# Kernel optimization log

Measured on AMD Instinct MI355X. Metric: run time of the kernel, lower is better.

Reference implementation:

```python
import jax, jax.numpy as jnp
import numpy as np

B, T, I, H, L = 128, 512, 64, 512, 64  # batch, seq_len, input=latent size, hidden
DEC_STEPS = 100  # hardcoded in the original decoder loop


def _lstm_cell(x, h, c, Wih, Whh, bih, bhh):
    # PyTorch gate order: i, f, g, o
    gates = x @ Wih.T + h @ Whh.T + bih + bhh  # [B, 4H]
    i, f, g, o = jnp.split(gates, 4, axis=-1)
    c = jax.nn.sigmoid(f) * c + jax.nn.sigmoid(i) * jnp.tanh(g)
    h = jax.nn.sigmoid(o) * jnp.tanh(c)
    return h, c


def setup_inputs() -> dict:
    key = jax.random.key(0)
    ks = jax.random.split(key, 18)
    u = lambda k, shape, fan: jax.random.uniform(k, shape, jnp.float32, -1.0, 1.0) / np.sqrt(fan).astype(np.float32)
    return {
        "sequences": jax.random.normal(ks[0], (B, T, I), jnp.float32),
        "seq_lengths": jnp.full((B,), T, dtype=jnp.int32),
        "eps": jax.random.normal(ks[1], (B, L), jnp.float32),
        "W_ih_enc": u(ks[2], (4 * H, I), H), "W_hh_enc": u(ks[3], (4 * H, H), H),
        "b_ih_enc": u(ks[4], (4 * H,), H), "b_hh_enc": u(ks[5], (4 * H,), H),
        "W_mean": u(ks[6], (L, H), H), "b_mean": u(ks[7], (L,), H),
        "W_logvar": u(ks[8], (L, H), H), "b_logvar": u(ks[9], (L,), H),
        "W_init": u(ks[10], (H, L), L), "b_init": u(ks[11], (H,), L),
        "W_ih_dec": u(ks[12], (4 * H, I), H), "W_hh_dec": u(ks[13], (4 * H, H), H),
        "b_ih_dec": u(ks[14], (4 * H,), H), "b_hh_dec": u(ks[15], (4 * H,), H),
        "W_out": u(ks[16], (I, H), H), "b_out": u(ks[17], (I,), H),
    }


def _forward(sequences, eps,
             W_ih_enc, W_hh_enc, b_ih_enc, b_hh_enc,
             W_mean, b_mean, W_logvar, b_logvar,
             W_init, b_init,
             W_ih_dec, W_hh_dec, b_ih_dec, b_hh_dec,
             W_out, b_out):
    Bn = sequences.shape[0]
    h0 = jnp.zeros((Bn, H), sequences.dtype)

    # ---- encoder: full-sequence LSTM, keep only final hidden state ----
    def enc_step(carry, x_t):
        h, c = carry
        h, c = _lstm_cell(x_t, h, c, W_ih_enc, W_hh_enc, b_ih_enc, b_hh_enc)
        return (h, c), None

    (h_n, _), _ = jax.lax.scan(enc_step, (h0, h0), sequences.transpose(1, 0, 2))

    # ---- VAE reparameterization ----
    mean = h_n @ W_mean.T + b_mean
    log_var = h_n @ W_logvar.T + b_logvar
    z = mean + eps * jnp.exp(0.5 * log_var)

    h_dec = z @ W_init.T + b_init
    c_dec = jnp.zeros_like(h_dec)
    x0 = jnp.zeros((Bn, L), z.dtype)

    def dec_step(carry, _):
        h, c, x = carry
        h, c = _lstm_cell(x, h, c, W_ih_dec, W_hh_dec, b_ih_dec, b_hh_dec)
        x_hat = h @ W_out.T + b_out
        return (h, c, x_hat), x_hat

    _, xs = jax.lax.scan(dec_step, (h_dec, c_dec, x0), None, length=DEC_STEPS)
    x_hat = xs.transpose(1, 0, 2)  # [B, 100, I]
    return x_hat, mean, log_var


def reference(sequences, seq_lengths, eps,
              W_ih_enc, W_hh_enc, b_ih_enc, b_hh_enc,
              W_mean, b_mean, W_logvar, b_logvar,
              W_init, b_init,
              W_ih_dec, W_hh_dec, b_ih_dec, b_hh_dec,
              W_out, b_out):
    del seq_lengths  # accepted but unused by the original forward
    return _forward(sequences, eps,
                    W_ih_enc, W_hh_enc, b_ih_enc, b_hh_enc,
                    W_mean, b_mean, W_logvar, b_logvar,
                    W_init, b_init,
                    W_ih_dec, W_hh_dec, b_ih_dec, b_hh_dec,
                    W_out, b_out)
```

## Files before the change

### kernel.cpp

```cpp
#include <hip/hip_runtime.h>
#include <stdint.h>


typedef short short8 __attribute__((ext_vector_type(8)));
typedef float f32x4 __attribute__((ext_vector_type(4)));
typedef unsigned int u32x4 __attribute__((ext_vector_type(4)));

#define WS_FLAGS  0
#define WS_HBUF0  16384
#define WS_HBUF1  147456
#define WS_Z      278528
#define WS_BCOMB  311296
#define WS_WCOMB  319488
#define WS_SEQB   2416640
#define WS_END    10805248
#define WS_ZERO   WS_HBUF1

static __device__ __forceinline__ float b2f(unsigned short u) {
    return __builtin_bit_cast(float, (unsigned int)u << 16);
}
static __device__ __forceinline__ unsigned short f2b(float f) {
    unsigned int u = __builtin_bit_cast(unsigned int, f);
    unsigned int r = u + 0x7FFFu + ((u >> 16) & 1u);
    return (unsigned short)(r >> 16);
}
static __device__ __forceinline__ float sigm(float x)  { return 1.0f / (1.0f + __expf(-x)); }
static __device__ __forceinline__ float tanhx(float x) { return 1.0f - 2.0f / (__expf(2.0f * x) + 1.0f); }

static __device__ __forceinline__ short8 cvt8(const float* p) {
    const float4 a = ((const float4*)p)[0];
    const float4 b = ((const float4*)p)[1];
    short8 r;
    r[0] = (short)f2b(a.x); r[1] = (short)f2b(a.y);
    r[2] = (short)f2b(a.z); r[3] = (short)f2b(a.w);
    r[4] = (short)f2b(b.x); r[5] = (short)f2b(b.y);
    r[6] = (short)f2b(b.z); r[7] = (short)f2b(b.w);
    return r;
}

static __device__ __forceinline__ void load2x16_cc(const void* p0, const void* p1,
                                                   u32x4& v0, u32x4& v1) {
    asm volatile("global_load_dwordx4 %0, %2, off sc0 sc1\n\t"
                 "global_load_dwordx4 %1, %3, off sc0 sc1\n\t"
                 "s_waitcnt vmcnt(0)"
                 : "=&v"(v0), "=&v"(v1) : "v"(p0), "v"(p1) : "memory");
}
static __device__ __forceinline__ void store16_cc(void* p, u32x4 v) {
    asm volatile("global_store_dwordx4 %0, %1, off sc0 sc1"
                 :: "v"(p), "v"(v) : "memory");
}
static __device__ __forceinline__ void drain_vm() {
    asm volatile("s_waitcnt vmcnt(0)" ::: "memory");
}

__global__ void __launch_bounds__(256)
seqcvt_kernel(const float* __restrict__ src, unsigned short* __restrict__ dst)
{
    int i = (blockIdx.x * 256 + threadIdx.x) * 4;
    float4 v = *(const float4*)(src + i);
    uint32_t lo = (uint32_t)f2b(v.x) | ((uint32_t)f2b(v.y) << 16);
    uint32_t hi = (uint32_t)f2b(v.z) | ((uint32_t)f2b(v.w) << 16);
    uint2 o; o.x = lo; o.y = hi;
    *(uint2*)(dst + i) = o;
}

__global__ void __launch_bounds__(256)
wcomb_kernel(const float* __restrict__ Wih_d,
             const float* __restrict__ Whh_d,
             const float* __restrict__ Wout,
             const float* __restrict__ bih_d,
             const float* __restrict__ bhh_d,
             const float* __restrict__ bout,
             unsigned char* __restrict__ ws)
{
    __shared__ float Ash[64][64];
    __shared__ float Bsh[64][65];
    const int bid = blockIdx.x, t = threadIdx.x;
    const int gt0 = (bid >> 3) * 64, ht0 = (bid & 7) * 64;
    for (int j = 0; j < 16; ++j) {
        int idx = t + j * 256;
        int r = idx >> 6, c = idx & 63;
        Ash[r][c] = Wih_d[(size_t)(gt0 + r) * 64 + c];
        Bsh[r][c] = Wout[(size_t)r * 512 + ht0 + c];
    }
    __syncthreads();
    const int gl = t >> 2, hl0 = (t & 3) * 16;
    for (int hh = 0; hh < 16; ++hh) {
        float acc = 0.f;
        #pragma unroll
        for (int i = 0; i < 64; ++i) acc += Ash[gl][i] * Bsh[i][hl0 + hh];
        int g = gt0 + gl, h = ht0 + hl0 + hh;
        float v = Whh_d[(size_t)g * 512 + h] + acc;
        ((unsigned short*)(ws + WS_WCOMB))[(size_t)g * 512 + h] = f2b(v);
    }
    if ((bid & 7) == 0 && t < 64) {
        int g = gt0 + t;
        float acc = bih_d[g] + bhh_d[g];
        #pragma unroll
        for (int i = 0; i < 64; ++i) acc += bout[i] * Ash[t][i];
        ((float*)(ws + WS_BCOMB))[g] = acc;
    }
}

__global__ void __launch_bounds__(512, 2)
vae_persistent(const float* __restrict__ seq,
               const unsigned short* __restrict__ seqb,
               const float* __restrict__ eps,
               const float* __restrict__ Wih_e,
               const float* __restrict__ Whh_e,
               const float* __restrict__ bih_e,
               const float* __restrict__ bhh_e,
               const float* __restrict__ Wmean,
               const float* __restrict__ bmean,
               const float* __restrict__ Wlv,
               const float* __restrict__ blv,
               const float* __restrict__ Winit,
               const float* __restrict__ binit,
               const float* __restrict__ Whh_d,
               const float* __restrict__ bih_d,
               const float* __restrict__ bhh_d,
               const float* __restrict__ Wout,
               const float* __restrict__ bout,
               unsigned char* __restrict__ ws,
               float* __restrict__ out)
{
    __shared__ __align__(16) short Al[16 * 520];
    __shared__ __align__(16) short Ho[512];
    __shared__ float fbuf[128];
    __shared__ float zl[16 * 64];

    const int tid  = threadIdx.x;
    const int g    = blockIdx.x & 7;
    const int s    = blockIdx.x >> 3;
    const int b0   = g * 16;
    const int lane = tid & 63;
    const int wv   = tid >> 6;
    const int col  = lane & 15;
    const int q    = lane >> 4;
    const int nloc = wv * 16 + col;
    const int gt   = nloc & 3;
    const int grow = gt * 512 + s * 32 + (nloc >> 2);

    uint32_t* flags = (uint32_t*)(ws + WS_FLAGS) + (size_t)g * 512;
    unsigned char* hbuf0 = ws + WS_HBUF0;
    unsigned char* hbuf1 = ws + WS_HBUF1;
    uint32_t* zbuf = (uint32_t*)(ws + WS_Z);

    float cst[4] = {0.f, 0.f, 0.f, 0.f};

    auto wait_and_stage = [&](uint32_t R) {
        if (wv == 0 && lane < 16) {
            while (__hip_atomic_load(&flags[lane * 32], __ATOMIC_RELAXED,
                                     __HIP_MEMORY_SCOPE_AGENT) < R) {}
        }
        __syncthreads();
        const unsigned char* src = (R & 1) ? hbuf1 : hbuf0;
        const int b = tid >> 5, c = tid & 31;
        const unsigned char* p0 = src + (size_t)(b0 + b) * 1024 + c * 32;
        u32x4 v0, v1;
        load2x16_cc(p0, p0 + 16, v0, v1);
        u32x4* dst = (u32x4*)Al;
        dst[b * 65 + c * 2 + 0] = v0;
        dst[b * 65 + c * 2 + 1] = v1;
        __syncthreads();
    };

    auto publish_h = [&](uint32_t R) {
        if (wv == 0) {
            unsigned char* dst = (R & 1) ? hbuf1 : hbuf0;
            int row = lane >> 2, part = lane & 3;
            u32x4 v = ((const u32x4*)Ho)[lane];
            store16_cc(dst + (size_t)(b0 + row) * 1024 + s * 64 + part * 16, v);
            drain_vm();
            if (lane == 0)
                __hip_atomic_store(&flags[s * 32], R, __ATOMIC_RELAXED,
                                   __HIP_MEMORY_SCOPE_AGENT);
        }
    };

    short8 wfrag[16];
    auto load_wfrag_f32 = [&](const float* Wsrc) {
        #pragma unroll
        for (int kt = 0; kt < 16; ++kt)
            wfrag[kt] = cvt8(Wsrc + (size_t)grow * 512 + kt * 32 + q * 8);
    };
    auto load_wfrag_bf16 = [&](const unsigned short* Wsrc) {
        #pragma unroll
        for (int kt = 0; kt < 16; ++kt)
            wfrag[kt] = *(const short8*)((const short*)Wsrc +
                         (size_t)grow * 512 + kt * 32 + q * 8);
    };

    auto cell_update = [&](f32x4 acc) {
        float act[4];
        #pragma unroll
        for (int r = 0; r < 4; ++r)
            act[r] = (gt == 2) ? tanhx(acc[r]) : sigm(acc[r]);
        int base = lane & ~3;
        #pragma unroll
        for (int r = 0; r < 4; ++r) {
            float vi = __shfl(act[r], base + 0);
            float vf = __shfl(act[r], base + 1);
            float vg = __shfl(act[r], base + 2);
            float vo = __shfl(act[r], base + 3);
            cst[r] = vf * cst[r] + vi * vg;
            act[r] = vo * tanhx(cst[r]);
        }
        if (gt == 0) {
            int hd4 = wv * 4 + (col >> 2);
            #pragma unroll
            for (int r = 0; r < 4; ++r)
                Ho[(q * 4 + r) * 32 + hd4] = (short)f2b(act[r]);
        }
    };

    load_wfrag_f32(Whh_e);
    short8 xwf[2];
    #pragma unroll
    for (int kt = 0; kt < 2; ++kt)
        xwf[kt] = cvt8(Wih_e + (size_t)grow * 64 + kt * 32 + q * 8);
    const float bias_e = bih_e[grow] + bhh_e[grow];

    auto load_x = [&](int t, short8* xf) {
        if (seqb) {
            const short* xs = (const short*)seqb + ((size_t)(b0 + col) * 512 + t) * 64 + q * 8;
            xf[0] = *(const short8*)(xs);
            xf[1] = *(const short8*)(xs + 32);
        } else {
            const float* xs = seq + ((size_t)(b0 + col) * 512 + t) * 64 + q * 8;
            xf[0] = cvt8(xs);
            xf[1] = cvt8(xs + 32);
        }
    };

    short8 xf[2];
    load_x(0, xf);
    for (uint32_t t = 0; t < 512; ++t) {
        wait_and_stage(t);
        f32x4 acc = {bias_e, bias_e, bias_e, bias_e};
        acc = __builtin_amdgcn_mfma_f32_16x16x32_bf16(xf[0], xwf[0], acc, 0, 0, 0);
        acc = __builtin_amdgcn_mfma_f32_16x16x32_bf16(xf[1], xwf[1], acc, 0, 0, 0);
        if (t < 511) load_x(t + 1, xf);
        #pragma unroll
        for (int kt = 0; kt < 16; ++kt) {
            short8 a = *(const short8*)(Al + col * 520 + kt * 32 + q * 8);
            acc = __builtin_amdgcn_mfma_f32_16x16x32_bf16(a, wfrag[kt], acc, 0, 0, 0);
        }
        cell_update(acc);
        __syncthreads();
        publish_h(t + 1);
    }

    wait_and_stage(512);
    if (tid < 128) {
        int which = tid >> 6, idx = tid & 63;
        int b = idx >> 2, ldl = idx & 3;
        int ld = s * 4 + ldl;
        const float* wrow = (which ? Wlv : Wmean) + (size_t)ld * 512;
        float a = (which ? blv[ld] : bmean[ld]);
        for (int k = 0; k < 512; ++k)
            a += b2f((unsigned short)Al[b * 520 + k]) * wrow[k];
        out[819200 + which * 8192 + (size_t)(b0 + b) * 64 + ld] = a;
        fbuf[which * 64 + idx] = a;
    }
    __syncthreads();
    if (wv == 0) {
        int b = lane >> 2, ldl = lane & 3;
        int ld = s * 4 + ldl;
        float m = fbuf[lane], lv = fbuf[64 + lane];
        float e = eps[(size_t)(b0 + b) * 64 + ld];
        float z = m + e * __expf(0.5f * lv);
        __hip_atomic_store(zbuf + (size_t)(b0 + b) * 64 + ld,
                           __builtin_bit_cast(uint32_t, z),
                           __ATOMIC_RELAXED, __HIP_MEMORY_SCOPE_AGENT);
        drain_vm();
        if (lane == 0)
            __hip_atomic_store(&flags[s * 32], 513u,
                               __ATOMIC_RELAXED, __HIP_MEMORY_SCOPE_AGENT);
    }
    if (wv == 0 && lane < 16)
        while (__hip_atomic_load(&flags[lane * 32], __ATOMIC_RELAXED,
                                 __HIP_MEMORY_SCOPE_AGENT) < 513u) {}
    __syncthreads();

    #pragma unroll
    for (int j = 0; j < 2; ++j) {
        int idx = tid + j * 512;
        int b = idx >> 6, l = idx & 63;
        uint32_t v = __hip_atomic_load(zbuf + (size_t)(b0 + b) * 64 + l,
                                       __ATOMIC_RELAXED, __HIP_MEMORY_SCOPE_AGENT);
        zl[b * 64 + l] = __builtin_bit_cast(float, v);
    }
    __syncthreads();
    {
        int b = tid >> 5, c = tid & 31;
        #pragma unroll
        for (int j = 0; j < 16; ++j) {
            int hd = c * 16 + j;
            float a = binit[hd];
            const float* wr = Winit + (size_t)hd * 64;
            #pragma unroll
            for (int l = 0; l < 64; ++l) a += zl[b * 64 + l] * wr[l];
            Al[b * 520 + hd] = (short)f2b(a);
        }
    }
    #pragma unroll
    for (int r = 0; r < 4; ++r) cst[r] = 0.f;
    __syncthreads();

    short8 wof[16];
    float xbias = 0.f;
    if (s < 4 && wv == 7) {
        xbias = bout[s * 16 + col];
        #pragma unroll
        for (int kt = 0; kt < 16; ++kt)
            wof[kt] = cvt8(Wout + (size_t)(s * 16 + col) * 512 + kt * 32 + q * 8);
    }
    auto xhat_emit = [&](int d) {
        f32x4 a2 = {xbias, xbias, xbias, xbias};
        #pragma unroll
        for (int kt = 0; kt < 16; ++kt) {
            short8 a = *(const short8*)(Al + col * 520 + kt * 32 + q * 8);
            a2 = __builtin_amdgcn_mfma_f32_16x16x32_bf16(a, wof[kt], a2, 0, 0, 0);
        }
        #pragma unroll
        for (int r = 0; r < 4; ++r) {
            int b = q * 4 + r;
            out[((size_t)(b0 + b) * 100 + d) * 64 + s * 16 + col] = a2[r];
        }
    };

    load_wfrag_f32(Whh_d);
    float bias = bih_d[grow] + bhh_d[grow];
    for (uint32_t d = 0; d < 100; ++d) {
        if (d > 0) wait_and_stage(513 + d);
        f32x4 acc = {bias, bias, bias, bias};
        #pragma unroll
        for (int kt = 0; kt < 16; ++kt) {
            short8 a = *(const short8*)(Al + col * 520 + kt * 32 + q * 8);
            acc = __builtin_amdgcn_mfma_f32_16x16x32_bf16(a, wfrag[kt], acc, 0, 0, 0);
        }
        cell_update(acc);
        __syncthreads();
        publish_h(514 + d);
        if (d >= 1 && s < 4 && wv == 7) xhat_emit(d - 1);
        if (d == 0) {
            load_wfrag_bf16((const unsigned short*)(ws + WS_WCOMB));
            bias = ((const float*)(ws + WS_BCOMB))[grow];
        }
    }
    wait_and_stage(613);
    if (s < 4 && wv == 7) xhat_emit(99);
}

extern "C" void kernel_launch(void* const* d_in, const int* in_sizes, int n_in,
                              void* d_out, int out_size, void* d_ws, size_t ws_size,
                              hipStream_t stream) {
    (void)in_sizes; (void)n_in; (void)out_size;
    const float* seq   = (const float*)d_in[0];
    const float* eps   = (const float*)d_in[2];
    const float* Wih_e = (const float*)d_in[3];
    const float* Whh_e = (const float*)d_in[4];
    const float* bih_e = (const float*)d_in[5];
    const float* bhh_e = (const float*)d_in[6];
    const float* Wmean = (const float*)d_in[7];
    const float* bmean = (const float*)d_in[8];
    const float* Wlv   = (const float*)d_in[9];
    const float* blv   = (const float*)d_in[10];
    const float* Winit = (const float*)d_in[11];
    const float* binit = (const float*)d_in[12];
    const float* Wih_d = (const float*)d_in[13];
    const float* Whh_d = (const float*)d_in[14];
    const float* bih_d = (const float*)d_in[15];
    const float* bhh_d = (const float*)d_in[16];
    const float* Wout  = (const float*)d_in[17];
    const float* bout  = (const float*)d_in[18];
    unsigned char* ws = (unsigned char*)d_ws;
    float* out = (float*)d_out;

    const bool have_seqb = ws_size >= (size_t)WS_END;
    unsigned short* seqb = have_seqb ? (unsigned short*)(ws + WS_SEQB) : nullptr;

    hipMemsetAsync(ws, 0, WS_ZERO, stream);
    if (have_seqb)
        seqcvt_kernel<<<4096, 256, 0, stream>>>(seq, seqb);
    wcomb_kernel<<<256, 256, 0, stream>>>(Wih_d, Whh_d, Wout, bih_d, bhh_d, bout, ws);
    vae_persistent<<<128, 512, 0, stream>>>(
        seq, seqb, eps, Wih_e, Whh_e, bih_e, bhh_e,
        Wmean, bmean, Wlv, blv, Winit, binit,
        Whh_d, bih_d, bhh_d, Wout, bout, ws, out);
}
```

Measured before the change: 2.014 ms.

## Replace flag-based inter-block sync with phase bits embedded in h data

```diff
diff --git a/kernel.cpp b/kernel.cpp
--- a/kernel.cpp
+++ b/kernel.cpp
@@ -15,6 +15,7 @@
 #define WS_SEQB   2416640
 #define WS_END    10805248
 #define WS_ZERO   WS_HBUF1
+#define HB1_SIZE  131072
 
 static __device__ __forceinline__ float b2f(unsigned short u) {
     return __builtin_bit_cast(float, (unsigned int)u << 16);
@@ -36,6 +37,11 @@
     r[4] = (short)f2b(b.x); r[5] = (short)f2b(b.y);
     r[6] = (short)f2b(b.z); r[7] = (short)f2b(b.w);
     return r;
+}
+
+static __device__ __forceinline__ uint32_t phase_of(uint32_t R) {
+    return (R <= 512u) ? ((R >> 1) & 1u)
+                       : ((((R - 513u) >> 1) & 1u) ^ 1u);
 }
 
 static __device__ __forceinline__ void load2x16_cc(const void* p0, const void* p1,
@@ -148,17 +154,25 @@
 
     float cst[4] = {0.f, 0.f, 0.f, 0.f};
 
-    auto wait_and_stage = [&](uint32_t R) {
-        if (wv == 0 && lane < 16) {
-            while (__hip_atomic_load(&flags[lane * 32], __ATOMIC_RELAXED,
-                                     __HIP_MEMORY_SCOPE_AGENT) < R) {}
-        }
-        __syncthreads();
+    auto wait_and_stage = [&](uint32_t R, bool guard) {
+        if (guard) __syncthreads();
         const unsigned char* src = (R & 1) ? hbuf1 : hbuf0;
+        const uint32_t pm = phase_of(R) ? 0x40004000u : 0u;
         const int b = tid >> 5, c = tid & 31;
         const unsigned char* p0 = src + (size_t)(b0 + b) * 1024 + c * 32;
         u32x4 v0, v1;
-        load2x16_cc(p0, p0 + 16, v0, v1);
+        for (;;) {
+            load2x16_cc(p0, p0 + 16, v0, v1);
+            uint32_t acc = 0;
+            #pragma unroll
+            for (int i = 0; i < 4; ++i) {
+                acc |= (v0[i] & 0x40004000u) ^ pm;
+                acc |= (v1[i] & 0x40004000u) ^ pm;
+            }
+            if (acc == 0) break;
+        }
+        #pragma unroll
+        for (int i = 0; i < 4; ++i) { v0[i] ^= pm; v1[i] ^= pm; }
         u32x4* dst = (u32x4*)Al;
         dst[b * 65 + c * 2 + 0] = v0;
         dst[b * 65 + c * 2 + 1] = v1;
@@ -168,13 +182,12 @@
     auto publish_h = [&](uint32_t R) {
         if (wv == 0) {
             unsigned char* dst = (R & 1) ? hbuf1 : hbuf0;
+            const uint32_t pm = phase_of(R) ? 0x40004000u : 0u;
             int row = lane >> 2, part = lane & 3;
             u32x4 v = ((const u32x4*)Ho)[lane];
+            #pragma unroll
+            for (int i = 0; i < 4; ++i) v[i] ^= pm;
             store16_cc(dst + (size_t)(b0 + row) * 1024 + s * 64 + part * 16, v);
-            drain_vm();
-            if (lane == 0)
-                __hip_atomic_store(&flags[s * 32], R, __ATOMIC_RELAXED,
-                                   __HIP_MEMORY_SCOPE_AGENT);
         }
     };
 
@@ -236,7 +249,7 @@
     short8 xf[2];
     load_x(0, xf);
     for (uint32_t t = 0; t < 512; ++t) {
-        wait_and_stage(t);
+        wait_and_stage(t, false);
         f32x4 acc = {bias_e, bias_e, bias_e, bias_e};
         acc = __builtin_amdgcn_mfma_f32_16x16x32_bf16(xf[0], xwf[0], acc, 0, 0, 0);
         acc = __builtin_amdgcn_mfma_f32_16x16x32_bf16(xf[1], xwf[1], acc, 0, 0, 0);
@@ -251,7 +264,7 @@
         publish_h(t + 1);
     }
 
-    wait_and_stage(512);
+    wait_and_stage(512, false);
     if (tid < 128) {
         int which = tid >> 6, idx = tid & 63;
         int b = idx >> 2, ldl = idx & 3;
@@ -333,7 +346,7 @@
     load_wfrag_f32(Whh_d);
     float bias = bih_d[grow] + bhh_d[grow];
     for (uint32_t d = 0; d < 100; ++d) {
-        if (d > 0) wait_and_stage(513 + d);
+        if (d > 0) wait_and_stage(513 + d, true);
         f32x4 acc = {bias, bias, bias, bias};
         #pragma unroll
         for (int kt = 0; kt < 16; ++kt) {
@@ -349,7 +362,7 @@
             bias = ((const float*)(ws + WS_BCOMB))[grow];
         }
     }
-    wait_and_stage(613);
+    wait_and_stage(613, true);
     if (s < 4 && wv == 7) xhat_emit(99);
 }
 
@@ -382,6 +395,7 @@
     unsigned short* seqb = have_seqb ? (unsigned short*)(ws + WS_SEQB) : nullptr;
 
     hipMemsetAsync(ws, 0, WS_ZERO, stream);
+    hipMemsetAsync(ws + WS_HBUF1, 0x40, HB1_SIZE, stream);
     if (have_seqb)
         seqcvt_kernel<<<4096, 256, 0, stream>>>(seq, seqb);
     wcomb_kernel<<<256, 256, 0, stream>>>(Wih_d, Whh_d, Wout, bih_d, bhh_d, bout, ws);
```

Result: slower. 2.457 ms (+22.0%).
